# Kernel tuning notes

Hardware: AMD Instinct MI355X
Metric: run time of the kernel (lower is better)

## Reference

```python
import jax, jax.numpy as jnp
import numpy as np

N_Q, N_T, D, C = 4096, 8192, 512, 16
SIGMA = 2.0


def setup_inputs() -> dict:
    key = jax.random.key(0)
    k1, k2, k3 = jax.random.split(key, 3)
    X = jax.random.normal(k1, (N_Q, D), dtype=jnp.float32)
    X_train = jax.random.normal(k2, (N_T, D), dtype=jnp.float32)
    y = jax.random.randint(k3, (N_T,), 0, C, dtype=jnp.int32)
    sigma = jnp.float32(SIGMA)
    return {"X": X, "X_train": X_train, "y": y, "sigma": sigma}


def reference(X, X_train, y, sigma):
    xx = jnp.sum(X * X, axis=1, keepdims=True)              # [N_q, 1]
    tt = jnp.sum(X_train * X_train, axis=1)                 # [N_t]
    cross = jnp.einsum('qd,td->qt', X, X_train)             # [N_q, N_t]
    dist2 = jnp.maximum(xx + tt[None, :] - 2.0 * cross, 0.0)
    pattern = jnp.exp(-dist2 / (2.0 * sigma ** 2))          # Gaussian RBF kernel [N_q, N_t]
    # per-class segment sum over training patterns (replaces per-class Python loop)
    summation = jax.ops.segment_sum(pattern.T, y, num_segments=C).T  # [N_q, C]
    summation = summation / jnp.sum(summation, axis=1, keepdims=True)
    return jnp.argmax(summation, axis=1)
```

## Files before the change

### kernel.cpp

```cpp
#include <hip/hip_runtime.h>


#define NQ 4096
#define NT 8192
#define DD 512
#define NC 16
#define LN_FLT_MIN -87.336544750402f
#define SCREEN_T 730.0f

typedef __attribute__((ext_vector_type(4))) int   v4i;
typedef __attribute__((ext_vector_type(8))) int   v8i;
typedef __attribute__((ext_vector_type(16))) float f32x16;

__global__ __launch_bounds__(256) void prep_k(const float* __restrict__ X,
                                              const float* __restrict__ XT,
                                              unsigned char* __restrict__ fX,
                                              unsigned char* __restrict__ fT,
                                              float* __restrict__ xx,
                                              float* __restrict__ tt,
                                              float* __restrict__ classacc) {
  const int lane = threadIdx.x & 63;
  const int row  = blockIdx.x * 4 + (threadIdx.x >> 6);
  const float* src; unsigned char* dst; float* nrm;
  if (row < NT) { src = XT + (size_t)row * DD; dst = fT + (size_t)row * DD; nrm = tt + row; }
  else { const int r = row - NT; src = X + (size_t)r * DD; dst = fX + (size_t)r * DD; nrm = xx + r; }
  const float4* s4 = (const float4*)src;
  const float4 a = s4[lane * 2], b = s4[lane * 2 + 1];
  int w0 = __builtin_amdgcn_cvt_pk_fp8_f32(a.x, a.y, 0, false);
  w0     = __builtin_amdgcn_cvt_pk_fp8_f32(a.z, a.w, w0, true);
  int w1 = __builtin_amdgcn_cvt_pk_fp8_f32(b.x, b.y, 0, false);
  w1     = __builtin_amdgcn_cvt_pk_fp8_f32(b.z, b.w, w1, true);
  int2 o; o.x = w0; o.y = w1;
  *(int2*)(dst + lane * 8) = o;
  float acc = a.x*a.x + a.y*a.y + a.z*a.z + a.w*a.w
            + b.x*b.x + b.y*b.y + b.z*b.z + b.w*b.w;
  #pragma unroll
  for (int off = 32; off; off >>= 1) acc += __shfl_down(acc, off, 64);
  if (lane == 0) *nrm = acc;
  if (blockIdx.x < 64) {
    float4 z = {0.f, 0.f, 0.f, 0.f};
    ((float4*)classacc)[blockIdx.x * 256 + threadIdx.x] = z;
  }
}

static __device__ __forceinline__ void stage_unit(const unsigned char* __restrict__ src,
                                                  int rowbase, int colbyte,
                                                  char* unitbase, int tid) {
  #pragma unroll
  for (int i = 0; i < 2; ++i) {
    const int row = i * 128 + (tid >> 2);
    const int sl  = (tid & 3) ^ ((row >> 1) & 3);
    const unsigned char* gp = src + (size_t)(rowbase + row) * DD + colbyte + sl * 16;
    __builtin_amdgcn_global_load_lds(
        (const __attribute__((address_space(1))) unsigned int*)gp,
        (__attribute__((address_space(3))) unsigned int*)(unitbase + i * 8192 + (tid >> 6) * 1024),
        16, 0, 0);
  }
}

static __device__ __forceinline__ v8i read32(const char* base, int off) {
  v4i lo = *(const v4i*)(base + off);
  v4i hi = *(const v4i*)(base + (off ^ 16));
  return __builtin_shufflevector(lo, hi, 0, 1, 2, 3, 4, 5, 6, 7);
}

#define BAR() __builtin_amdgcn_s_barrier()
#define WAITV(N) asm volatile("s_waitcnt vmcnt(" #N ")" ::: "memory")

__global__ __launch_bounds__(512, 2) void pnn_mfma(const unsigned char* __restrict__ fX,
                                                   const unsigned char* __restrict__ fT,
                                                   const float* __restrict__ Xf,
                                                   const float* __restrict__ Tf,
                                                   const int* __restrict__ y,
                                                   const float* __restrict__ sigp,
                                                   const float* __restrict__ xx,
                                                   const float* __restrict__ tt,
                                                   float* __restrict__ classacc) {
  extern __shared__ char lds[];
  const int tid  = threadIdx.x;
  const int w    = tid >> 6, lane = tid & 63;
  const int wr   = w >> 2, wc = w & 3;
  const int la   = lane & 31, lb = lane >> 5;

  const int bid = blockIdx.x;
  const int xcd = bid & 7, c = bid >> 3;
  const int qt = (xcd & 1) * 8 + (c >> 3);
  const int tn = (xcd >> 1) * 8 + (c & 7);
  const int qbase = qt * 256, tbase = tn * 256;

  char* const A0 = lds;
  char* const A1 = lds + 32768;
  char* const B0 = lds + 65536;
  char* const B1 = lds + 98304;

  const int g   = (la >> 1) & 3;
  const int p0  = (((lb * 2) ^ g) * 16);
  const int arow = (wr * 128 + la) * 64;
  const int brow = (wc * 64 + la) * 64;

  stage_unit(fX, qbase, 0,   A0,         tid);
  stage_unit(fT, tbase, 0,   B0,         tid);
  stage_unit(fX, qbase, 64,  A0 + 16384, tid);
  stage_unit(fT, tbase, 64,  B0 + 16384, tid);
  stage_unit(fX, qbase, 128, A1,         tid);
  stage_unit(fT, tbase, 128, B1,         tid);
  WAITV(8);
  __builtin_amdgcn_sched_barrier(0);
  BAR();

  f32x16 acc[4][2];
  #pragma unroll
  for (int mt = 0; mt < 4; ++mt)
    #pragma unroll
    for (int nt = 0; nt < 2; ++nt) acc[mt][nt] = (f32x16)(0.0f);

  char* cA = A0; char* cB = B0; char* nA = A1; char* nB = B1;

#define PHASE(ABASE, BBASE, STAGE_STMT, WAIT_STMT)                             \
  {                                                                            \
    v8i af[4], bfr[2];                                                         \
    _Pragma("unroll")                                                          \
    for (int mt = 0; mt < 4; ++mt) af[mt] = read32((ABASE), arow + mt * 2048 + p0); \
    _Pragma("unroll")                                                          \
    for (int nt = 0; nt < 2; ++nt) bfr[nt] = read32((BBASE), brow + nt * 2048 + p0); \
    STAGE_STMT                                                                 \
    BAR();                                                                     \
    __builtin_amdgcn_s_setprio(1);                                             \
    _Pragma("unroll")                                                          \
    for (int mt = 0; mt < 4; ++mt)                                             \
      _Pragma("unroll")                                                        \
      for (int nt = 0; nt < 2; ++nt)                                           \
        acc[mt][nt] = __builtin_amdgcn_mfma_scale_f32_32x32x64_f8f6f4(         \
            af[mt], bfr[nt], acc[mt][nt], 0, 0, 0, 127, 0, 127);               \
    __builtin_amdgcn_s_setprio(0);                                             \
    WAIT_STMT                                                                  \
    BAR();                                                                     \
  }

  for (int kt = 0; kt < 4; ++kt) {
    PHASE(cA, cB,
          { if (kt < 3) { stage_unit(fX, qbase, (2 * kt + 3) * 64, nA + 16384, tid);
                          stage_unit(fT, tbase, (2 * kt + 3) * 64, nB + 16384, tid); } },
          { if (kt < 3) { WAITV(8); } else { WAITV(0); } })
    PHASE(cA + 16384, cB + 16384,
          { if (kt < 2) { stage_unit(fX, qbase, (2 * kt + 4) * 64, cA, tid);
                          stage_unit(fT, tbase, (2 * kt + 4) * 64, cB, tid); } },
          { if (kt < 2) { WAITV(8); } else if (kt == 2) { WAITV(4); } })
    char* t0 = cA; cA = nA; nA = t0;
    char* t1 = cB; cB = nB; nB = t1;
  }
#undef PHASE

  const float sg = sigp[0];
  const float inv2s2 = 1.0f / (2.0f * sg * sg);
  const int qb = qbase + wr * 128;
  const int tbc = tbase + wc * 64;
  float tnorm[2]; int tcls[2];
  #pragma unroll
  for (int nt = 0; nt < 2; ++nt) {
    const int t = tbc + nt * 32 + la;
    tnorm[nt] = tt[t]; tcls[nt] = y[t];
  }
  #pragma unroll
  for (int mt = 0; mt < 4; ++mt) {
    #pragma unroll
    for (int reg = 0; reg < 16; ++reg) {
      const int q = qb + mt * 32 + (reg & 3) + 8 * (reg >> 2) + 4 * lb;
      const float xq = xx[q];
      #pragma unroll
      for (int nt = 0; nt < 2; ++nt) {
        const float d2 = xq + tnorm[nt] - 2.0f * acc[mt][nt][reg];
        if (__builtin_expect(d2 < SCREEN_T, 0)) {
          const int t = tbc + nt * 32 + la;
          const float4* xp = (const float4*)(Xf + (size_t)q * DD);
          const float4* tp = (const float4*)(Tf + (size_t)t * DD);
          float s0 = 0.f, s1 = 0.f, s2 = 0.f, s3 = 0.f;
          for (int d = 0; d < DD / 4; ++d) {
            const float4 xv = xp[d], tv = tp[d];
            s0 = fmaf(xv.x, tv.x, s0); s1 = fmaf(xv.y, tv.y, s1);
            s2 = fmaf(xv.z, tv.z, s2); s3 = fmaf(xv.w, tv.w, s3);
          }
          const float dot = (s0 + s1) + (s2 + s3);
          const float dd2 = fmaxf(xq + tnorm[nt] - 2.0f * dot, 0.f);
          const float arg = -dd2 * inv2s2;
          if (arg >= LN_FLT_MIN)
            atomicAdd(&classacc[q * NC + tcls[nt]], expf(arg));
        }
      }
    }
  }
}

__global__ __launch_bounds__(256) void argmax_k(const float* __restrict__ classacc,
                                                float* __restrict__ out) {
  const int q = blockIdx.x * 256 + threadIdx.x;
  float sc[NC];
  #pragma unroll
  for (int c4 = 0; c4 < 4; ++c4) {
    const float4 v = ((const float4*)(classacc + (size_t)q * NC))[c4];
    sc[c4*4+0] = v.x; sc[c4*4+1] = v.y; sc[c4*4+2] = v.z; sc[c4*4+3] = v.w;
  }
  float rowsum = 0.f;
  #pragma unroll
  for (int c = 0; c < NC; ++c) rowsum += sc[c];
  int best = 0; float bv = sc[0];
  #pragma unroll
  for (int c = 1; c < NC; ++c)
    if (sc[c] > bv) { bv = sc[c]; best = c; }
  out[q] = (rowsum > 0.f) ? (float)best : 0.0f;
}

extern "C" void kernel_launch(void* const* d_in, const int* in_sizes, int n_in,
                              void* d_out, int out_size, void* d_ws, size_t ws_size,
                              hipStream_t stream) {
  const float* X  = (const float*)d_in[0];
  const float* XT = (const float*)d_in[1];
  const int*   y  = (const int*)d_in[2];
  const float* sg = (const float*)d_in[3];
  float* out = (float*)d_out;

  char* wsp = (char*)d_ws;
  unsigned char* fX = (unsigned char*)wsp;
  unsigned char* fT = fX + (size_t)NQ * DD;
  float* tt       = (float*)(wsp + 8u * 1024u * 1024u);
  float* xx       = tt + NT;
  float* classacc = xx + NQ;

  (void)hipFuncSetAttribute((const void*)pnn_mfma,
                            hipFuncAttributeMaxDynamicSharedMemorySize, 131072);

  prep_k<<<(NQ + NT) / 4, 256, 0, stream>>>(X, XT, fX, fT, xx, tt, classacc);
  pnn_mfma<<<512, 512, 131072, stream>>>(fX, fT, X, XT, y, sg, xx, tt, classacc);
  argmax_k<<<NQ / 256, 256, 0, stream>>>(classacc, out);
}
```

Baseline: 47.02 us.

## Shrink MFMA block tile to 128x256 with double-buffered K=64 stages for occupancy

Cuts the query tile per block from 256 to 128 rows, doubling the grid to 1024 blocks. LDS drops to about 50KB per block so launch bounds can target 4 blocks per CU. The deep multi-stage pipeline is replaced with a simpler double buffer that waits on all loads and hits a barrier every K step. Query norms, train norms and labels are cached in LDS for the epilogue. The aim is to hide latency through more resident waves, at the cost of re-reading train data more often and syncing more frequently.

```diff
diff --git a/kernel.cpp b/kernel.cpp
--- a/kernel.cpp
+++ b/kernel.cpp
@@ -43,9 +43,20 @@
   }
 }
 
-static __device__ __forceinline__ void stage_unit(const unsigned char* __restrict__ src,
-                                                  int rowbase, int colbyte,
-                                                  char* unitbase, int tid) {
+static __device__ __forceinline__ void stageA(const unsigned char* __restrict__ src,
+                                              int rowbase, int colbyte,
+                                              char* unit, int tid) {
+  const int row = tid >> 2;
+  const int sl  = (tid & 3) ^ ((row >> 1) & 3);
+  const unsigned char* gp = src + (size_t)(rowbase + row) * DD + colbyte + sl * 16;
+  __builtin_amdgcn_global_load_lds(
+      (const __attribute__((address_space(1))) unsigned int*)gp,
+      (__attribute__((address_space(3))) unsigned int*)(unit + (tid >> 6) * 1024),
+      16, 0, 0);
+}
+static __device__ __forceinline__ void stageB(const unsigned char* __restrict__ src,
+                                              int rowbase, int colbyte,
+                                              char* unit, int tid) {
   #pragma unroll
   for (int i = 0; i < 2; ++i) {
     const int row = i * 128 + (tid >> 2);
@@ -53,7 +64,7 @@
     const unsigned char* gp = src + (size_t)(rowbase + row) * DD + colbyte + sl * 16;
     __builtin_amdgcn_global_load_lds(
         (const __attribute__((address_space(1))) unsigned int*)gp,
-        (__attribute__((address_space(3))) unsigned int*)(unitbase + i * 8192 + (tid >> 6) * 1024),
+        (__attribute__((address_space(3))) unsigned int*)(unit + i * 8192 + (tid >> 6) * 1024),
         16, 0, 0);
   }
 }
@@ -65,9 +76,9 @@
 }
 
 #define BAR() __builtin_amdgcn_s_barrier()
-#define WAITV(N) asm volatile("s_waitcnt vmcnt(" #N ")" ::: "memory")
-
-__global__ __launch_bounds__(512, 2) void pnn_mfma(const unsigned char* __restrict__ fX,
+#define WAITV0() asm volatile("s_waitcnt vmcnt(0)" ::: "memory")
+
+__global__ __launch_bounds__(512, 4) void pnn_mfma(const unsigned char* __restrict__ fX,
                                                    const unsigned char* __restrict__ fT,
                                                    const float* __restrict__ Xf,
                                                    const float* __restrict__ Tf,
@@ -77,101 +88,86 @@
                                                    const float* __restrict__ tt,
                                                    float* __restrict__ classacc) {
   extern __shared__ char lds[];
+  char* const A0 = lds;
+  char* const A1 = lds + 8192;
+  char* const B0 = lds + 16384;
+  char* const B1 = lds + 32768;
+  float* const xxs = (float*)(lds + 49152);
+  float* const tts = (float*)(lds + 49664);
+  int*   const ycl = (int*)  (lds + 50688);
+
   const int tid  = threadIdx.x;
   const int w    = tid >> 6, lane = tid & 63;
   const int wr   = w >> 2, wc = w & 3;
   const int la   = lane & 31, lb = lane >> 5;
 
   const int bid = blockIdx.x;
-  const int xcd = bid & 7, c = bid >> 3;
-  const int qt = (xcd & 1) * 8 + (c >> 3);
-  const int tn = (xcd >> 1) * 8 + (c & 7);
-  const int qbase = qt * 256, tbase = tn * 256;
-
-  char* const A0 = lds;
-  char* const A1 = lds + 32768;
-  char* const B0 = lds + 65536;
-  char* const B1 = lds + 98304;
-
-  const int g   = (la >> 1) & 3;
-  const int p0  = (((lb * 2) ^ g) * 16);
-  const int arow = (wr * 128 + la) * 64;
+  const int xcd = bid & 7, cc = bid >> 3;
+  const int qt = (xcd & 3) * 8 + (cc >> 4);
+  const int tn = (xcd >> 2) * 16 + (cc & 15);
+  const int qbase = qt * 128, tbase = tn * 256;
+
+  const int g    = (la >> 1) & 3;
+  const int p0   = ((lb * 2) ^ g) * 16;
+  const int arow = (wr * 64 + la) * 64;
   const int brow = (wc * 64 + la) * 64;
 
-  stage_unit(fX, qbase, 0,   A0,         tid);
-  stage_unit(fT, tbase, 0,   B0,         tid);
-  stage_unit(fX, qbase, 64,  A0 + 16384, tid);
-  stage_unit(fT, tbase, 64,  B0 + 16384, tid);
-  stage_unit(fX, qbase, 128, A1,         tid);
-  stage_unit(fT, tbase, 128, B1,         tid);
-  WAITV(8);
-  __builtin_amdgcn_sched_barrier(0);
-  BAR();
-
-  f32x16 acc[4][2];
-  #pragma unroll
-  for (int mt = 0; mt < 4; ++mt)
+  if (tid < 128) xxs[tid] = xx[qbase + tid];
+  if (tid < 256) { tts[tid] = tt[tbase + tid]; ycl[tid] = y[tbase + tid]; }
+
+  stageA(fX, qbase, 0, A0, tid);
+  stageB(fT, tbase, 0, B0, tid);
+  __syncthreads();
+
+  f32x16 acc[2][2];
+  #pragma unroll
+  for (int mt = 0; mt < 2; ++mt)
     #pragma unroll
     for (int nt = 0; nt < 2; ++nt) acc[mt][nt] = (f32x16)(0.0f);
 
   char* cA = A0; char* cB = B0; char* nA = A1; char* nB = B1;
 
-#define PHASE(ABASE, BBASE, STAGE_STMT, WAIT_STMT)                             \
-  {                                                                            \
-    v8i af[4], bfr[2];                                                         \
-    _Pragma("unroll")                                                          \
-    for (int mt = 0; mt < 4; ++mt) af[mt] = read32((ABASE), arow + mt * 2048 + p0); \
-    _Pragma("unroll")                                                          \
-    for (int nt = 0; nt < 2; ++nt) bfr[nt] = read32((BBASE), brow + nt * 2048 + p0); \
-    STAGE_STMT                                                                 \
-    BAR();                                                                     \
-    __builtin_amdgcn_s_setprio(1);                                             \
-    _Pragma("unroll")                                                          \
-    for (int mt = 0; mt < 4; ++mt)                                             \
-      _Pragma("unroll")                                                        \
-      for (int nt = 0; nt < 2; ++nt)                                           \
-        acc[mt][nt] = __builtin_amdgcn_mfma_scale_f32_32x32x64_f8f6f4(         \
-            af[mt], bfr[nt], acc[mt][nt], 0, 0, 0, 127, 0, 127);               \
-    __builtin_amdgcn_s_setprio(0);                                             \
-    WAIT_STMT                                                                  \
-    BAR();                                                                     \
-  }
-
-  for (int kt = 0; kt < 4; ++kt) {
-    PHASE(cA, cB,
-          { if (kt < 3) { stage_unit(fX, qbase, (2 * kt + 3) * 64, nA + 16384, tid);
-                          stage_unit(fT, tbase, (2 * kt + 3) * 64, nB + 16384, tid); } },
-          { if (kt < 3) { WAITV(8); } else { WAITV(0); } })
-    PHASE(cA + 16384, cB + 16384,
-          { if (kt < 2) { stage_unit(fX, qbase, (2 * kt + 4) * 64, cA, tid);
-                          stage_unit(fT, tbase, (2 * kt + 4) * 64, cB, tid); } },
-          { if (kt < 2) { WAITV(8); } else if (kt == 2) { WAITV(4); } })
+  for (int kt = 0; kt < 8; ++kt) {
+    if (kt < 7) {
+      stageA(fX, qbase, (kt + 1) * 64, nA, tid);
+      stageB(fT, tbase, (kt + 1) * 64, nB, tid);
+    }
+    v8i af0 = read32(cA, arow + p0);
+    v8i af1 = read32(cA, arow + 2048 + p0);
+    v8i bf0 = read32(cB, brow + p0);
+    v8i bf1 = read32(cB, brow + 2048 + p0);
+    __builtin_amdgcn_s_setprio(1);
+    acc[0][0] = __builtin_amdgcn_mfma_scale_f32_32x32x64_f8f6f4(af0, bf0, acc[0][0], 0, 0, 0, 127, 0, 127);
+    acc[0][1] = __builtin_amdgcn_mfma_scale_f32_32x32x64_f8f6f4(af0, bf1, acc[0][1], 0, 0, 0, 127, 0, 127);
+    acc[1][0] = __builtin_amdgcn_mfma_scale_f32_32x32x64_f8f6f4(af1, bf0, acc[1][0], 0, 0, 0, 127, 0, 127);
+    acc[1][1] = __builtin_amdgcn_mfma_scale_f32_32x32x64_f8f6f4(af1, bf1, acc[1][1], 0, 0, 0, 127, 0, 127);
+    __builtin_amdgcn_s_setprio(0);
+    WAITV0();
+    BAR();
     char* t0 = cA; cA = nA; nA = t0;
     char* t1 = cB; cB = nB; nB = t1;
   }
-#undef PHASE
 
   const float sg = sigp[0];
   const float inv2s2 = 1.0f / (2.0f * sg * sg);
-  const int qb = qbase + wr * 128;
-  const int tbc = tbase + wc * 64;
   float tnorm[2]; int tcls[2];
   #pragma unroll
   for (int nt = 0; nt < 2; ++nt) {
-    const int t = tbc + nt * 32 + la;
-    tnorm[nt] = tt[t]; tcls[nt] = y[t];
-  }
-  #pragma unroll
-  for (int mt = 0; mt < 4; ++mt) {
+    const int tl = wc * 64 + nt * 32 + la;
+    tnorm[nt] = tts[tl]; tcls[nt] = ycl[tl];
+  }
+  #pragma unroll
+  for (int mt = 0; mt < 2; ++mt) {
     #pragma unroll
     for (int reg = 0; reg < 16; ++reg) {
-      const int q = qb + mt * 32 + (reg & 3) + 8 * (reg >> 2) + 4 * lb;
-      const float xq = xx[q];
+      const int ql = wr * 64 + mt * 32 + (reg & 3) + 8 * (reg >> 2) + 4 * lb;
+      const float xq = xxs[ql];
       #pragma unroll
       for (int nt = 0; nt < 2; ++nt) {
         const float d2 = xq + tnorm[nt] - 2.0f * acc[mt][nt][reg];
         if (__builtin_expect(d2 < SCREEN_T, 0)) {
-          const int t = tbc + nt * 32 + la;
+          const int q = qbase + ql;
+          const int t = tbase + wc * 64 + nt * 32 + la;
           const float4* xp = (const float4*)(Xf + (size_t)q * DD);
           const float4* tp = (const float4*)(Tf + (size_t)t * DD);
           float s0 = 0.f, s1 = 0.f, s2 = 0.f, s3 = 0.f;
@@ -227,9 +223,9 @@
   float* classacc = xx + NQ;
 
   (void)hipFuncSetAttribute((const void*)pnn_mfma,
-                            hipFuncAttributeMaxDynamicSharedMemorySize, 131072);
+                            hipFuncAttributeMaxDynamicSharedMemorySize, 51712);
 
   prep_k<<<(NQ + NT) / 4, 256, 0, stream>>>(X, XT, fX, fT, xx, tt, classacc);
-  pnn_mfma<<<512, 512, 131072, stream>>>(fX, fT, X, XT, y, sg, xx, tt, classacc);
+  pnn_mfma<<<1024, 512, 51712, stream>>>(fX, fT, X, XT, y, sg, xx, tt, classacc);
   argmax_k<<<NQ / 256, 256, 0, stream>>>(classacc, out);
 }
```

After: 160.7 us. 3.42x slower.
